# Performance work log

Hardware: AMD Instinct MI355X
Metric: run time of the kernel (lower is better)

Reference implementation:

```python
import jax, jax.numpy as jnp
import numpy as np

PI_APPROX = 3.14  # the original module uses 3.14, not math.pi
FPS = 30.0        # hard-coded sampling rate in calc_hr_torch


def setup_inputs() -> dict:
    key = jax.random.key(0)
    x = jax.random.normal(key, (4096, 4096), dtype=jnp.float32)
    return {"x": x}


def reference(x) -> jnp.ndarray:
    test_n, sig_length = x.shape
    # mean-subtract each signal (over last dim)
    x = x - jnp.mean(x, axis=-1, keepdims=True)

    # custom_fft: DFT over dim 0 (size test_n), O(N^2) via trig matmuls
    N = test_n
    n = jnp.arange(N, dtype=jnp.float32)[:, None]  # [N,1]
    k = jnp.arange(N, dtype=jnp.float32)[None, :]  # [1,N]
    ang = (-2.0 * PI_APPROX / N) * (k * n)         # [N,N]
    real_part = jnp.matmul(jnp.cos(ang), x)        # [N, sig_length]
    imag_part = jnp.matmul(jnp.sin(ang), x)

    # custom_rfft: keep non-negative frequencies along dim 0
    half = N // 2 + 1 if N % 2 == 0 else (N + 1) // 2
    real_part = real_part[:half]
    imag_part = imag_part[:half]

    Ns = sig_length
    freq = jnp.arange(Ns, dtype=jnp.float32) / (Ns / FPS)  # [sig_length]
    amplitude = jnp.sqrt(real_part ** 2 + imag_part ** 2) / Ns  # [half, sig_length]
    hr_list = freq[jnp.argmax(amplitude, axis=-1)] * 60.0       # [half]
    return hr_list
```

## Files before the change

### kernel.cpp

```cpp
#include <hip/hip_runtime.h>
#include <cmath>

typedef _Float16 f16;
typedef _Float16 f16x8 __attribute__((ext_vector_type(8)));
typedef float f32x4 __attribute__((ext_vector_type(4)));
typedef unsigned long long u64;

#define M_OUT 2049
#define NDIM 4096
#define MPAD 2112
#define CW ((float)(-2.0 * 3.14 / 4096.0))

static const size_t WS_MEAN  = 0;
static const size_t WS_CELLS = 16384;
static const size_t WS_TBL   = 40960;
static const size_t A_ELEMS  = (size_t)MPAD * NDIM;
static const size_t X_ELEMS  = (size_t)NDIM * NDIM;
static const size_t WS_XTBL  = WS_TBL + 4 * A_ELEMS * sizeof(f16);
static const size_t WS_FULL_END = WS_XTBL + 2 * X_ELEMS * sizeof(f16);
static const size_t WS_MID_END  = WS_TBL + 4 * A_ELEMS * sizeof(f16);

#define AS1 __attribute__((address_space(1)))
#define AS3 __attribute__((address_space(3)))
__device__ __forceinline__ void async_copy16(const void* gsrc, void* ldst) {
    __builtin_amdgcn_global_load_lds((const AS1 unsigned int*)gsrc,
                                     (AS3 unsigned int*)ldst, 16, 0, 0);
}

__device__ __forceinline__ void split_f16(float v, f16& hi, f16& lo) {
    hi = (f16)v;
    lo = (f16)((v - (float)hi) * 64.0f);
}

__global__ void mean_kernel(const float* __restrict__ x, float* __restrict__ meanv) {
    const int row = blockIdx.x;
    const float4* xr = (const float4*)(x + (size_t)row * NDIM);
    float s = 0.f;
    for (int i = threadIdx.x; i < NDIM / 4; i += 256) {
        float4 v = xr[i];
        s += (v.x + v.y) + (v.z + v.w);
    }
    for (int off = 32; off; off >>= 1) s += __shfl_down(s, off);
    __shared__ float ps[4];
    if ((threadIdx.x & 63) == 0) ps[threadIdx.x >> 6] = s;
    __syncthreads();
    if (threadIdx.x == 0) {
        float t = (ps[0] + ps[1]) + (ps[2] + ps[3]);
        meanv[row] = t * (1.0f / 4096.0f);
    }
}

__global__ void init_cells(u64* __restrict__ cells) {
    int i = blockIdx.x * 256 + threadIdx.x;
    if (i < M_OUT) cells[i] = 0ull;
}

__global__ void fill_A_cm(f16* __restrict__ tbl) {
    const int c = blockIdx.x;
    const int m = blockIdx.y * 256 + threadIdx.x;
    if (m >= MPAD) return;
    const bool valid = (m < M_OUT);
    f16x8 chv, clv, shv, slv;
    for (int j = 0; j < 8; ++j) {
        float cc = 0.f, ss = 0.f;
        if (valid) {
            int kk = c * 8 + j;
            float ang = CW * (float)(m * kk);
            sincosf(ang, &ss, &cc);
        }
        f16 h, l;
        split_f16(cc, h, l); chv[j] = h; clv[j] = l;
        split_f16(ss, h, l); shv[j] = h; slv[j] = l;
    }
    size_t idx = ((size_t)c * MPAD + m) * 8;
    *(f16x8*)(tbl + idx)                 = chv;
    *(f16x8*)(tbl + A_ELEMS + idx)       = clv;
    *(f16x8*)(tbl + 2 * A_ELEMS + idx)   = shv;
    *(f16x8*)(tbl + 3 * A_ELEMS + idx)   = slv;
}

__global__ void fill_X_cm(const float* __restrict__ x, const float* __restrict__ meanv,
                          f16* __restrict__ xtbl) {
    const int c = blockIdx.x;
    const int n = blockIdx.y * 256 + threadIdx.x;
    f16x8 hv, lv;
    for (int j = 0; j < 8; ++j) {
        int k = c * 8 + j;
        float v = x[(size_t)k * NDIM + n] - meanv[k];
        f16 h, l;
        split_f16(v, h, l);
        hv[j] = h; lv[j] = l;
    }
    size_t idx = ((size_t)c * NDIM + n) * 8;
    *(f16x8*)(xtbl + idx)           = hv;
    *(f16x8*)(xtbl + X_ELEMS + idx) = lv;
}

__global__ __launch_bounds__(256, 2) void dft_gemm_cm(
    const f16* __restrict__ atbl, const f16* __restrict__ xtbl,
    u64* __restrict__ cells)
{
    __shared__ alignas(16) f16 sX[3][2][4][128][8];

    const int t = threadIdx.x;
    const int n0      = blockIdx.x * 128;
    const int rowBase = blockIdx.y * 64;

    const int lane = t & 63;
    const int w  = t >> 6;
    const int wm = w >> 1, wn = w & 1;
    const int q  = lane >> 4, ln = lane & 15;

    f32x4 aC0[2][4], aC1[2][4], aS0[2][4], aS1[2][4];
#pragma unroll
    for (int i = 0; i < 2; ++i)
#pragma unroll
        for (int j = 0; j < 4; ++j) {
            aC0[i][j] = (f32x4){0.f, 0.f, 0.f, 0.f};
            aC1[i][j] = (f32x4){0.f, 0.f, 0.f, 0.f};
            aS0[i][j] = (f32x4){0.f, 0.f, 0.f, 0.f};
            aS1[i][j] = (f32x4){0.f, 0.f, 0.f, 0.f};
        }

    const f16* aBase = atbl + ((size_t)q * MPAD + (rowBase + wm * 32 + ln)) * 8;

    const int xq0 = w >> 1, xh = w & 1;
    const int xq1 = xq0 + 2;
    const f16* xG0 = xtbl + ((size_t)xq0 * NDIM + n0 + xh * 64 + lane) * 8;
    const f16* xG1 = xtbl + ((size_t)xq1 * NDIM + n0 + xh * 64 + lane) * 8;
    const f16* xG2 = xG0 + X_ELEMS;
    const f16* xG3 = xG1 + X_ELEMS;

    auto loadA = [&](f16x8 (&dst)[2][4], int kc) {
#pragma unroll
        for (int tm = 0; tm < 2; ++tm)
#pragma unroll
            for (int tb = 0; tb < 4; ++tb)
                dst[tm][tb] = *(const f16x8*)(aBase + (size_t)tb * A_ELEMS
                              + ((size_t)kc * MPAD + tm * 16) * 8);
    };

    auto stageX = [&](int buf, int kc) {
        const size_t kadv = (size_t)kc * NDIM * 8;
        async_copy16(xG0 + kadv, &sX[buf][0][xq0][xh * 64][0]);
        async_copy16(xG1 + kadv, &sX[buf][0][xq1][xh * 64][0]);
        async_copy16(xG2 + kadv, &sX[buf][1][xq0][xh * 64][0]);
        async_copy16(xG3 + kadv, &sX[buf][1][xq1][xh * 64][0]);
    };

    auto compute = [&](f16x8 (&A)[2][4], int buf) {
        f16x8 bh[4], bl[4];
#pragma unroll
        for (int tn = 0; tn < 4; ++tn) {
            int nl = wn * 64 + tn * 16 + ln;
            bh[tn] = *(const f16x8*)&sX[buf][0][q][nl][0];
            bl[tn] = *(const f16x8*)&sX[buf][1][q][nl][0];
        }
        __builtin_amdgcn_s_setprio(1);
#pragma unroll
        for (int tm = 0; tm < 2; ++tm)
#pragma unroll
            for (int tn = 0; tn < 4; ++tn) {
                aC0[tm][tn] = __builtin_amdgcn_mfma_f32_16x16x32_f16(A[tm][0], bh[tn], aC0[tm][tn], 0, 0, 0);
                aC1[tm][tn] = __builtin_amdgcn_mfma_f32_16x16x32_f16(A[tm][0], bl[tn], aC1[tm][tn], 0, 0, 0);
                aC1[tm][tn] = __builtin_amdgcn_mfma_f32_16x16x32_f16(A[tm][1], bh[tn], aC1[tm][tn], 0, 0, 0);
                aS0[tm][tn] = __builtin_amdgcn_mfma_f32_16x16x32_f16(A[tm][2], bh[tn], aS0[tm][tn], 0, 0, 0);
                aS1[tm][tn] = __builtin_amdgcn_mfma_f32_16x16x32_f16(A[tm][2], bl[tn], aS1[tm][tn], 0, 0, 0);
                aS1[tm][tn] = __builtin_amdgcn_mfma_f32_16x16x32_f16(A[tm][3], bh[tn], aS1[tm][tn], 0, 0, 0);
            }
        __builtin_amdgcn_s_setprio(0);
    };

    f16x8 Aa[2][4], Ab[2][4];
    int cur = 0, nxt = 1;
    auto bump = [&]() { cur = nxt; nxt = (nxt == 2) ? 0 : nxt + 1; };

    stageX(0, 0);
    loadA(Aa, 0);

    int kc = 0;
    for (int it = 0; it < 63; ++it) {
        loadA(Ab, kc + 4);
        stageX(nxt, kc + 4);
        asm volatile("s_waitcnt vmcnt(12)" ::: "memory");
        __builtin_amdgcn_s_barrier();
        __builtin_amdgcn_sched_barrier(0);
        compute(Aa, cur);
        bump();
        kc += 4;
        loadA(Aa, kc + 4);
        stageX(nxt, kc + 4);
        asm volatile("s_waitcnt vmcnt(12)" ::: "memory");
        __builtin_amdgcn_s_barrier();
        __builtin_amdgcn_sched_barrier(0);
        compute(Ab, cur);
        bump();
        kc += 4;
    }
    loadA(Ab, kc + 4);
    stageX(nxt, kc + 4);
    asm volatile("s_waitcnt vmcnt(12)" ::: "memory");
    __builtin_amdgcn_s_barrier();
    __builtin_amdgcn_sched_barrier(0);
    compute(Aa, cur);
    bump();
    asm volatile("s_waitcnt vmcnt(0)" ::: "memory");
    __builtin_amdgcn_s_barrier();
    __builtin_amdgcn_sched_barrier(0);
    compute(Ab, cur);

    const float inv64 = 0.015625f;
#pragma unroll
    for (int tm = 0; tm < 2; ++tm) {
#pragma unroll
        for (int r = 0; r < 4; ++r) {
            u64 best = 0ull;
#pragma unroll
            for (int tn = 0; tn < 4; ++tn) {
                float C = aC0[tm][tn][r] + aC1[tm][tn][r] * inv64;
                float S = aS0[tm][tn][r] + aS1[tm][tn][r] * inv64;
                float a2 = C * C + S * S;
                int col = n0 + wn * 64 + tn * 16 + ln;
                u64 key = ((u64)__float_as_uint(a2) << 32) | (unsigned)(~col);
                if (key > best) best = key;
            }
            for (int off = 1; off < 16; off <<= 1) {
                unsigned hi = (unsigned)(best >> 32), lo = (unsigned)best;
                unsigned ho = __shfl_xor(hi, off);
                unsigned lo2 = __shfl_xor(lo, off);
                u64 o = ((u64)ho << 32) | lo2;
                if (o > best) best = o;
            }
            if (ln == 0) {
                int grow = rowBase + wm * 32 + tm * 16 + q * 4 + r;
                if (grow < M_OUT) atomicMax(cells + grow, best);
            }
        }
    }
}

__global__ void fill_tables_rm(f16* __restrict__ tbl) {
    long long g = (long long)blockIdx.x * 256 + threadIdx.x;
    if (g >= (long long)(MPAD * 512)) return;
    int m  = (int)(g >> 9);
    int kq = ((int)g & 511) * 8;
    bool valid = (m < M_OUT);
    f16x8 chv, clv, shv, slv;
    for (int j = 0; j < 8; ++j) {
        float c = 0.f, s = 0.f;
        if (valid) {
            int kk = kq + j;
            float ang = CW * (float)(m * kk);
            sincosf(ang, &s, &c);
        }
        f16 h, l;
        split_f16(c, h, l); chv[j] = h; clv[j] = l;
        split_f16(s, h, l); shv[j] = h; slv[j] = l;
    }
    size_t idx = (size_t)m * NDIM + kq;
    *(f16x8*)(tbl + idx)               = chv;
    *(f16x8*)(tbl + A_ELEMS + idx)     = clv;
    *(f16x8*)(tbl + 2 * A_ELEMS + idx) = shv;
    *(f16x8*)(tbl + 3 * A_ELEMS + idx) = slv;
}

#define PK 40
__global__ __launch_bounds__(256, 2) void dft_gemm_fb(
    const float* __restrict__ x, const float* __restrict__ meanv,
    const f16* __restrict__ tbl, int useTbl,
    u64* __restrict__ cells)
{
    __shared__ alignas(16) f16 Ach[64][PK];
    __shared__ alignas(16) f16 Acl[64][PK];
    __shared__ alignas(16) f16 Ash[64][PK];
    __shared__ alignas(16) f16 Asl[64][PK];
    __shared__ alignas(16) f16 Xh[128][PK];
    __shared__ alignas(16) f16 Xl[128][PK];

    const int t = threadIdx.x;
    const int n0      = blockIdx.x * 128;
    const int rowBase = blockIdx.y * 64;

    const int am  = t >> 2;
    const int akq = (t & 3) * 8;
    const int xn  = t & 127;
    const int xkh = (t >> 7) * 16;

    const int lane = t & 63;
    const int w  = t >> 6;
    const int wm = w >> 1, wn = w & 1;
    const int q  = lane >> 4, ln = lane & 15;

    f32x4 aC0[2][4], aC1[2][4], aS0[2][4], aS1[2][4];
    for (int i = 0; i < 2; ++i)
        for (int j = 0; j < 4; ++j) {
            aC0[i][j] = (f32x4){0.f, 0.f, 0.f, 0.f};
            aC1[i][j] = (f32x4){0.f, 0.f, 0.f, 0.f};
            aS0[i][j] = (f32x4){0.f, 0.f, 0.f, 0.f};
            aS1[i][j] = (f32x4){0.f, 0.f, 0.f, 0.f};
        }

    const int arow = rowBase + am;
    const bool avalid = (arow < M_OUT);

    for (int k0 = 0; k0 < NDIM; k0 += 32) {
        __syncthreads();
        if (useTbl) {
            size_t idx = (size_t)arow * NDIM + k0 + akq;
            *(f16x8*)&Ach[am][akq] = *(const f16x8*)(tbl + idx);
            *(f16x8*)&Acl[am][akq] = *(const f16x8*)(tbl + A_ELEMS + idx);
            *(f16x8*)&Ash[am][akq] = *(const f16x8*)(tbl + 2 * A_ELEMS + idx);
            *(f16x8*)&Asl[am][akq] = *(const f16x8*)(tbl + 3 * A_ELEMS + idx);
        } else {
            f16x8 chv, clv, shv, slv;
            for (int j = 0; j < 8; ++j) {
                float c = 0.f, s = 0.f;
                if (avalid) {
                    int kk = k0 + akq + j;
                    float ang = CW * (float)(arow * kk);
                    sincosf(ang, &s, &c);
                }
                f16 h, l;
                split_f16(c, h, l); chv[j] = h; clv[j] = l;
                split_f16(s, h, l); shv[j] = h; slv[j] = l;
            }
            *(f16x8*)&Ach[am][akq] = chv;
            *(f16x8*)&Acl[am][akq] = clv;
            *(f16x8*)&Ash[am][akq] = shv;
            *(f16x8*)&Asl[am][akq] = slv;
        }
        {
            const float* xp = x + (size_t)(k0 + xkh) * NDIM + n0 + xn;
            f16x8 h0, h1, l0, l1;
            for (int r = 0; r < 16; ++r) {
                float v = xp[(size_t)r * NDIM] - meanv[k0 + xkh + r];
                f16 hi, lo;
                split_f16(v, hi, lo);
                if (r < 8) { h0[r] = hi; l0[r] = lo; }
                else       { h1[r - 8] = hi; l1[r - 8] = lo; }
            }
            *(f16x8*)&Xh[xn][xkh]     = h0;
            *(f16x8*)&Xh[xn][xkh + 8] = h1;
            *(f16x8*)&Xl[xn][xkh]     = l0;
            *(f16x8*)&Xl[xn][xkh + 8] = l1;
        }
        __syncthreads();
        f16x8 fch[2], fcl[2], fsh[2], fsl[2], bh[4], bl[4];
        for (int tm = 0; tm < 2; ++tm) {
            int ml = wm * 32 + tm * 16 + ln;
            fch[tm] = *(const f16x8*)&Ach[ml][q * 8];
            fcl[tm] = *(const f16x8*)&Acl[ml][q * 8];
            fsh[tm] = *(const f16x8*)&Ash[ml][q * 8];
            fsl[tm] = *(const f16x8*)&Asl[ml][q * 8];
        }
        for (int tn = 0; tn < 4; ++tn) {
            int nl = wn * 64 + tn * 16 + ln;
            bh[tn] = *(const f16x8*)&Xh[nl][q * 8];
            bl[tn] = *(const f16x8*)&Xl[nl][q * 8];
        }
        for (int tm = 0; tm < 2; ++tm)
            for (int tn = 0; tn < 4; ++tn) {
                aC0[tm][tn] = __builtin_amdgcn_mfma_f32_16x16x32_f16(fch[tm], bh[tn], aC0[tm][tn], 0, 0, 0);
                aC1[tm][tn] = __builtin_amdgcn_mfma_f32_16x16x32_f16(fch[tm], bl[tn], aC1[tm][tn], 0, 0, 0);
                aC1[tm][tn] = __builtin_amdgcn_mfma_f32_16x16x32_f16(fcl[tm], bh[tn], aC1[tm][tn], 0, 0, 0);
                aS0[tm][tn] = __builtin_amdgcn_mfma_f32_16x16x32_f16(fsh[tm], bh[tn], aS0[tm][tn], 0, 0, 0);
                aS1[tm][tn] = __builtin_amdgcn_mfma_f32_16x16x32_f16(fsh[tm], bl[tn], aS1[tm][tn], 0, 0, 0);
                aS1[tm][tn] = __builtin_amdgcn_mfma_f32_16x16x32_f16(fsl[tm], bh[tn], aS1[tm][tn], 0, 0, 0);
            }
    }

    const float inv64 = 0.015625f;
    for (int tm = 0; tm < 2; ++tm) {
        for (int r = 0; r < 4; ++r) {
            u64 best = 0ull;
            for (int tn = 0; tn < 4; ++tn) {
                float C = aC0[tm][tn][r] + aC1[tm][tn][r] * inv64;
                float S = aS0[tm][tn][r] + aS1[tm][tn][r] * inv64;
                float a2 = C * C + S * S;
                int col = n0 + wn * 64 + tn * 16 + ln;
                u64 key = ((u64)__float_as_uint(a2) << 32) | (unsigned)(~col);
                if (key > best) best = key;
            }
            for (int off = 1; off < 16; off <<= 1) {
                unsigned hi = (unsigned)(best >> 32), lo = (unsigned)best;
                unsigned ho = __shfl_xor(hi, off);
                unsigned lo2 = __shfl_xor(lo, off);
                u64 o = ((u64)ho << 32) | lo2;
                if (o > best) best = o;
            }
            if (ln == 0) {
                int grow = rowBase + wm * 32 + tm * 16 + q * 4 + r;
                if (grow < M_OUT) atomicMax(cells + grow, best);
            }
        }
    }
}

__global__ void out_kernel(const u64* __restrict__ cells, float* __restrict__ out) {
    int i = blockIdx.x * 256 + threadIdx.x;
    if (i < M_OUT) {
        unsigned col = ~(unsigned)(cells[i] & 0xFFFFFFFFull);
        float freq = (float)col / (4096.0f / 30.0f);
        out[i] = freq * 60.0f;
    }
}

extern "C" void kernel_launch(void* const* d_in, const int* in_sizes, int n_in,
                              void* d_out, int out_size, void* d_ws, size_t ws_size,
                              hipStream_t stream) {
    const float* x = (const float*)d_in[0];
    char* ws = (char*)d_ws;
    float* meanv = (float*)(ws + WS_MEAN);
    u64*   cells = (u64*)(ws + WS_CELLS);
    f16*   atbl  = (f16*)(ws + WS_TBL);
    f16*   xtbl  = (f16*)(ws + WS_XTBL);
    float* out   = (float*)d_out;

    hipLaunchKernelGGL(init_cells, dim3((M_OUT + 255) / 256), dim3(256), 0, stream, cells);
    hipLaunchKernelGGL(mean_kernel, dim3(NDIM), dim3(256), 0, stream, x, meanv);

    if (ws_size >= WS_FULL_END) {
        hipLaunchKernelGGL(fill_A_cm, dim3(512, 9), dim3(256), 0, stream, atbl);
        hipLaunchKernelGGL(fill_X_cm, dim3(512, 16), dim3(256), 0, stream, x, meanv, xtbl);
        hipLaunchKernelGGL(dft_gemm_cm, dim3(32, 33), dim3(256), 0, stream, atbl, xtbl, cells);
    } else if (ws_size >= WS_MID_END) {
        hipLaunchKernelGGL(fill_tables_rm, dim3(4224), dim3(256), 0, stream, atbl);
        hipLaunchKernelGGL(dft_gemm_fb, dim3(32, 33), dim3(256), 0, stream,
                           x, meanv, atbl, 1, cells);
    } else {
        hipLaunchKernelGGL(dft_gemm_fb, dim3(32, 33), dim3(256), 0, stream,
                           x, meanv, atbl, 0, cells);
    }
    hipLaunchKernelGGL(out_kernel, dim3((M_OUT + 255) / 256), dim3(256), 0, stream, cells, out);
}
```

Baseline: 533.5 us.

## Merge prep kernels and fold tail row tile into first-row blocks

Zero-initialisation of the argmax cells moves into the mean kernel, and the two table-fill kernels become one launch, removing two kernel launches. The GEMM grid shrinks from 33 to 32 row tiles. Blocks with blockIdx.y==0 run a second pass covering the leftover tail rows (2048..2111), so the grid of 1024 blocks divides evenly across the CUs instead of leaving a nearly empty extra wave. The cost is that those 32 blocks take twice as long, which creates a tail imbalance of its own.

Measured after the change: 538.6 us. No clear change (+0.9%).

```diff
diff --git a/kernel.cpp b/kernel.cpp
--- a/kernel.cpp
+++ b/kernel.cpp
@@ -32,7 +32,12 @@
     lo = (f16)((v - (float)hi) * 64.0f);
 }
 
-__global__ void mean_kernel(const float* __restrict__ x, float* __restrict__ meanv) {
+__global__ void mean_kernel(const float* __restrict__ x, float* __restrict__ meanv,
+                            u64* __restrict__ cells) {
+    if (blockIdx.x < 9) {
+        int i = blockIdx.x * 256 + threadIdx.x;
+        if (i < M_OUT) cells[i] = 0ull;
+    }
     const int row = blockIdx.x;
     const float4* xr = (const float4*)(x + (size_t)row * NDIM);
     float s = 0.f;
@@ -50,50 +55,44 @@
     }
 }
 
-__global__ void init_cells(u64* __restrict__ cells) {
-    int i = blockIdx.x * 256 + threadIdx.x;
-    if (i < M_OUT) cells[i] = 0ull;
-}
-
-__global__ void fill_A_cm(f16* __restrict__ tbl) {
+__global__ void fill_tables_cm(const float* __restrict__ x, const float* __restrict__ meanv,
+                               f16* __restrict__ atbl, f16* __restrict__ xtbl) {
     const int c = blockIdx.x;
-    const int m = blockIdx.y * 256 + threadIdx.x;
-    if (m >= MPAD) return;
-    const bool valid = (m < M_OUT);
-    f16x8 chv, clv, shv, slv;
-    for (int j = 0; j < 8; ++j) {
-        float cc = 0.f, ss = 0.f;
-        if (valid) {
-            int kk = c * 8 + j;
-            float ang = CW * (float)(m * kk);
-            sincosf(ang, &ss, &cc);
-        }
-        f16 h, l;
-        split_f16(cc, h, l); chv[j] = h; clv[j] = l;
-        split_f16(ss, h, l); shv[j] = h; slv[j] = l;
-    }
-    size_t idx = ((size_t)c * MPAD + m) * 8;
-    *(f16x8*)(tbl + idx)                 = chv;
-    *(f16x8*)(tbl + A_ELEMS + idx)       = clv;
-    *(f16x8*)(tbl + 2 * A_ELEMS + idx)   = shv;
-    *(f16x8*)(tbl + 3 * A_ELEMS + idx)   = slv;
-}
-
-__global__ void fill_X_cm(const float* __restrict__ x, const float* __restrict__ meanv,
-                          f16* __restrict__ xtbl) {
-    const int c = blockIdx.x;
-    const int n = blockIdx.y * 256 + threadIdx.x;
-    f16x8 hv, lv;
-    for (int j = 0; j < 8; ++j) {
-        int k = c * 8 + j;
-        float v = x[(size_t)k * NDIM + n] - meanv[k];
-        f16 h, l;
-        split_f16(v, h, l);
-        hv[j] = h; lv[j] = l;
-    }
-    size_t idx = ((size_t)c * NDIM + n) * 8;
-    *(f16x8*)(xtbl + idx)           = hv;
-    *(f16x8*)(xtbl + X_ELEMS + idx) = lv;
+    if (blockIdx.y < 9) {
+        const int m = blockIdx.y * 256 + threadIdx.x;
+        if (m >= MPAD) return;
+        const bool valid = (m < M_OUT);
+        f16x8 chv, clv, shv, slv;
+        for (int j = 0; j < 8; ++j) {
+            float cc = 0.f, ss = 0.f;
+            if (valid) {
+                int kk = c * 8 + j;
+                float ang = CW * (float)(m * kk);
+                sincosf(ang, &ss, &cc);
+            }
+            f16 h, l;
+            split_f16(cc, h, l); chv[j] = h; clv[j] = l;
+            split_f16(ss, h, l); shv[j] = h; slv[j] = l;
+        }
+        size_t idx = ((size_t)c * MPAD + m) * 8;
+        *(f16x8*)(atbl + idx)                 = chv;
+        *(f16x8*)(atbl + A_ELEMS + idx)       = clv;
+        *(f16x8*)(atbl + 2 * A_ELEMS + idx)   = shv;
+        *(f16x8*)(atbl + 3 * A_ELEMS + idx)   = slv;
+    } else {
+        const int n = (blockIdx.y - 9) * 256 + threadIdx.x;
+        f16x8 hv, lv;
+        for (int j = 0; j < 8; ++j) {
+            int k = c * 8 + j;
+            float v = x[(size_t)k * NDIM + n] - meanv[k];
+            f16 h, l;
+            split_f16(v, h, l);
+            hv[j] = h; lv[j] = l;
+        }
+        size_t idx = ((size_t)c * NDIM + n) * 8;
+        *(f16x8*)(xtbl + idx)           = hv;
+        *(f16x8*)(xtbl + X_ELEMS + idx) = lv;
+    }
 }
 
 __global__ __launch_bounds__(256, 2) void dft_gemm_cm(
@@ -103,8 +102,8 @@
     __shared__ alignas(16) f16 sX[3][2][4][128][8];
 
     const int t = threadIdx.x;
-    const int n0      = blockIdx.x * 128;
-    const int rowBase = blockIdx.y * 64;
+    const int n0 = blockIdx.x * 128;
+    const int by = blockIdx.y;
 
     const int lane = t & 63;
     const int w  = t >> 6;
@@ -112,17 +111,6 @@
     const int q  = lane >> 4, ln = lane & 15;
 
     f32x4 aC0[2][4], aC1[2][4], aS0[2][4], aS1[2][4];
-#pragma unroll
-    for (int i = 0; i < 2; ++i)
-#pragma unroll
-        for (int j = 0; j < 4; ++j) {
-            aC0[i][j] = (f32x4){0.f, 0.f, 0.f, 0.f};
-            aC1[i][j] = (f32x4){0.f, 0.f, 0.f, 0.f};
-            aS0[i][j] = (f32x4){0.f, 0.f, 0.f, 0.f};
-            aS1[i][j] = (f32x4){0.f, 0.f, 0.f, 0.f};
-        }
-
-    const f16* aBase = atbl + ((size_t)q * MPAD + (rowBase + wm * 32 + ln)) * 8;
 
     const int xq0 = w >> 1, xh = w & 1;
     const int xq1 = xq0 + 2;
@@ -130,15 +118,6 @@
     const f16* xG1 = xtbl + ((size_t)xq1 * NDIM + n0 + xh * 64 + lane) * 8;
     const f16* xG2 = xG0 + X_ELEMS;
     const f16* xG3 = xG1 + X_ELEMS;
-
-    auto loadA = [&](f16x8 (&dst)[2][4], int kc) {
-#pragma unroll
-        for (int tm = 0; tm < 2; ++tm)
-#pragma unroll
-            for (int tb = 0; tb < 4; ++tb)
-                dst[tm][tb] = *(const f16x8*)(aBase + (size_t)tb * A_ELEMS
-                              + ((size_t)kc * MPAD + tm * 16) * 8);
-    };
 
     auto stageX = [&](int buf, int kc) {
         const size_t kadv = (size_t)kc * NDIM * 8;
@@ -172,14 +151,58 @@
     };
 
     f16x8 Aa[2][4], Ab[2][4];
-    int cur = 0, nxt = 1;
-    auto bump = [&]() { cur = nxt; nxt = (nxt == 2) ? 0 : nxt + 1; };
-
-    stageX(0, 0);
-    loadA(Aa, 0);
-
-    int kc = 0;
-    for (int it = 0; it < 63; ++it) {
+
+    const int npass = (by == 0) ? 2 : 1;
+    for (int pass = 0; pass < npass; ++pass) {
+        const int rowBase = (pass == 0) ? by * 64 : 2048;
+        __syncthreads();
+
+#pragma unroll
+        for (int i = 0; i < 2; ++i)
+#pragma unroll
+            for (int j = 0; j < 4; ++j) {
+                aC0[i][j] = (f32x4){0.f, 0.f, 0.f, 0.f};
+                aC1[i][j] = (f32x4){0.f, 0.f, 0.f, 0.f};
+                aS0[i][j] = (f32x4){0.f, 0.f, 0.f, 0.f};
+                aS1[i][j] = (f32x4){0.f, 0.f, 0.f, 0.f};
+            }
+
+        const f16* aBase = atbl + ((size_t)q * MPAD + (rowBase + wm * 32 + ln)) * 8;
+
+        auto loadA = [&](f16x8 (&dst)[2][4], int kc) {
+#pragma unroll
+            for (int tm = 0; tm < 2; ++tm)
+#pragma unroll
+                for (int tb = 0; tb < 4; ++tb)
+                    dst[tm][tb] = *(const f16x8*)(aBase + (size_t)tb * A_ELEMS
+                                  + ((size_t)kc * MPAD + tm * 16) * 8);
+        };
+
+        int cur = 0, nxt = 1;
+        auto bump = [&]() { cur = nxt; nxt = (nxt == 2) ? 0 : nxt + 1; };
+
+        stageX(0, 0);
+        loadA(Aa, 0);
+
+        int kc = 0;
+        for (int it = 0; it < 63; ++it) {
+            loadA(Ab, kc + 4);
+            stageX(nxt, kc + 4);
+            asm volatile("s_waitcnt vmcnt(12)" ::: "memory");
+            __builtin_amdgcn_s_barrier();
+            __builtin_amdgcn_sched_barrier(0);
+            compute(Aa, cur);
+            bump();
+            kc += 4;
+            loadA(Aa, kc + 4);
+            stageX(nxt, kc + 4);
+            asm volatile("s_waitcnt vmcnt(12)" ::: "memory");
+            __builtin_amdgcn_s_barrier();
+            __builtin_amdgcn_sched_barrier(0);
+            compute(Ab, cur);
+            bump();
+            kc += 4;
+        }
         loadA(Ab, kc + 4);
         stageX(nxt, kc + 4);
         asm volatile("s_waitcnt vmcnt(12)" ::: "memory");
@@ -187,53 +210,37 @@
         __builtin_amdgcn_sched_barrier(0);
         compute(Aa, cur);
         bump();
-        kc += 4;
-        loadA(Aa, kc + 4);
-        stageX(nxt, kc + 4);
-        asm volatile("s_waitcnt vmcnt(12)" ::: "memory");
+        asm volatile("s_waitcnt vmcnt(0)" ::: "memory");
         __builtin_amdgcn_s_barrier();
         __builtin_amdgcn_sched_barrier(0);
         compute(Ab, cur);
-        bump();
-        kc += 4;
-    }
-    loadA(Ab, kc + 4);
-    stageX(nxt, kc + 4);
-    asm volatile("s_waitcnt vmcnt(12)" ::: "memory");
-    __builtin_amdgcn_s_barrier();
-    __builtin_amdgcn_sched_barrier(0);
-    compute(Aa, cur);
-    bump();
-    asm volatile("s_waitcnt vmcnt(0)" ::: "memory");
-    __builtin_amdgcn_s_barrier();
-    __builtin_amdgcn_sched_barrier(0);
-    compute(Ab, cur);
-
-    const float inv64 = 0.015625f;
-#pragma unroll
-    for (int tm = 0; tm < 2; ++tm) {
-#pragma unroll
-        for (int r = 0; r < 4; ++r) {
-            u64 best = 0ull;
-#pragma unroll
-            for (int tn = 0; tn < 4; ++tn) {
-                float C = aC0[tm][tn][r] + aC1[tm][tn][r] * inv64;
-                float S = aS0[tm][tn][r] + aS1[tm][tn][r] * inv64;
-                float a2 = C * C + S * S;
-                int col = n0 + wn * 64 + tn * 16 + ln;
-                u64 key = ((u64)__float_as_uint(a2) << 32) | (unsigned)(~col);
-                if (key > best) best = key;
-            }
-            for (int off = 1; off < 16; off <<= 1) {
-                unsigned hi = (unsigned)(best >> 32), lo = (unsigned)best;
-                unsigned ho = __shfl_xor(hi, off);
-                unsigned lo2 = __shfl_xor(lo, off);
-                u64 o = ((u64)ho << 32) | lo2;
-                if (o > best) best = o;
-            }
-            if (ln == 0) {
-                int grow = rowBase + wm * 32 + tm * 16 + q * 4 + r;
-                if (grow < M_OUT) atomicMax(cells + grow, best);
+
+        const float inv64 = 0.015625f;
+#pragma unroll
+        for (int tm = 0; tm < 2; ++tm) {
+#pragma unroll
+            for (int r = 0; r < 4; ++r) {
+                u64 best = 0ull;
+#pragma unroll
+                for (int tn = 0; tn < 4; ++tn) {
+                    float C = aC0[tm][tn][r] + aC1[tm][tn][r] * inv64;
+                    float S = aS0[tm][tn][r] + aS1[tm][tn][r] * inv64;
+                    float a2 = C * C + S * S;
+                    int col = n0 + wn * 64 + tn * 16 + ln;
+                    u64 key = ((u64)__float_as_uint(a2) << 32) | (unsigned)(~col);
+                    if (key > best) best = key;
+                }
+                for (int off = 1; off < 16; off <<= 1) {
+                    unsigned hi = (unsigned)(best >> 32), lo = (unsigned)best;
+                    unsigned ho = __shfl_xor(hi, off);
+                    unsigned lo2 = __shfl_xor(lo, off);
+                    u64 o = ((u64)ho << 32) | lo2;
+                    if (o > best) best = o;
+                }
+                if (ln == 0) {
+                    int grow = rowBase + wm * 32 + tm * 16 + q * 4 + r;
+                    if (grow < M_OUT) atomicMax(cells + grow, best);
+                }
             }
         }
     }
@@ -416,13 +423,12 @@
     f16*   xtbl  = (f16*)(ws + WS_XTBL);
     float* out   = (float*)d_out;
 
-    hipLaunchKernelGGL(init_cells, dim3((M_OUT + 255) / 256), dim3(256), 0, stream, cells);
-    hipLaunchKernelGGL(mean_kernel, dim3(NDIM), dim3(256), 0, stream, x, meanv);
+    hipLaunchKernelGGL(mean_kernel, dim3(NDIM), dim3(256), 0, stream, x, meanv, cells);
 
     if (ws_size >= WS_FULL_END) {
-        hipLaunchKernelGGL(fill_A_cm, dim3(512, 9), dim3(256), 0, stream, atbl);
-        hipLaunchKernelGGL(fill_X_cm, dim3(512, 16), dim3(256), 0, stream, x, meanv, xtbl);
-        hipLaunchKernelGGL(dft_gemm_cm, dim3(32, 33), dim3(256), 0, stream, atbl, xtbl, cells);
+        hipLaunchKernelGGL(fill_tables_cm, dim3(512, 25), dim3(256), 0, stream,
+                           x, meanv, atbl, xtbl);
+        hipLaunchKernelGGL(dft_gemm_cm, dim3(32, 32), dim3(256), 0, stream, atbl, xtbl, cells);
     } else if (ws_size >= WS_MID_END) {
         hipLaunchKernelGGL(fill_tables_rm, dim3(4224), dim3(256), 0, stream, atbl);
         hipLaunchKernelGGL(dft_gemm_fb, dim3(32, 33), dim3(256), 0, stream,
```
